# Kernel tuning notes

Hardware: AMD Instinct MI355X
Metric: run time of the kernel (lower is better)

Reference implementation:

```python
import jax, jax.numpy as jnp
import numpy as np

B, T, F, H, C = 256, 128, 256, 512, 10


def setup_inputs() -> dict:
    key = jax.random.key(0)
    ks = jax.random.split(key, 11)
    s_in = 1.0 / np.sqrt(H)  # torch RNN init scale ~ U(-1/sqrt(H), 1/sqrt(H)); use scaled normal
    return {
        "x": jax.random.normal(ks[0], (B, T, F), jnp.float32),
        "W_ih0": jax.random.normal(ks[1], (H, F), jnp.float32) * s_in,
        "W_hh0": jax.random.normal(ks[2], (H, H), jnp.float32) * s_in,
        "b_ih0": jax.random.normal(ks[3], (H,), jnp.float32) * s_in,
        "b_hh0": jax.random.normal(ks[4], (H,), jnp.float32) * s_in,
        "W_ih1": jax.random.normal(ks[5], (H, H), jnp.float32) * s_in,
        "W_hh1": jax.random.normal(ks[6], (H, H), jnp.float32) * s_in,
        "b_ih1": jax.random.normal(ks[7], (H,), jnp.float32) * s_in,
        "b_hh1": jax.random.normal(ks[8], (H,), jnp.float32) * s_in,
        "W_fc": jax.random.normal(ks[9], (C, H * T), jnp.float32) * (1.0 / np.sqrt(H * T)),
        "b_fc": jax.random.normal(ks[10], (C,), jnp.float32) * 0.01,
    }


def _rnn_layer(inp, W_ih, W_hh, b_ih, b_hh):
    # inp: [B, T, Fin]. Precompute all input-to-hidden projections in one GEMM.
    proj = jnp.einsum('btf,hf->bth', inp, W_ih) + b_ih + b_hh  # [B, T, H]

    def step(h, p_t):
        h_new = jax.nn.relu(p_t + h @ W_hh.T)  # h_t = relu(x W_ih^T + b_ih + h_{t-1} W_hh^T + b_hh)
        return h_new, h_new

    h0 = jnp.zeros((inp.shape[0], W_hh.shape[0]), inp.dtype)
    _, outs = jax.lax.scan(step, h0, jnp.swapaxes(proj, 0, 1))  # scan over T
    return jnp.swapaxes(outs, 0, 1)  # [B, T, H]


def reference(x, W_ih0, W_hh0, b_ih0, b_hh0, W_ih1, W_hh1, b_ih1, b_hh1, W_fc, b_fc):
    h = _rnn_layer(x, W_ih0, W_hh0, b_ih0, b_hh0)
    h = _rnn_layer(h, W_ih1, W_hh1, b_ih1, b_hh1)
    flat = h.reshape(h.shape[0], -1)  # [B, T*H]
    return flat @ W_fc.T + b_fc  # [B, C]
```

## Files before the change

kernel.cpp:

```cpp
#include <hip/hip_runtime.h>
#include <cstddef>

#define B_ 256
#define T_ 128
#define F_ 256
#define H_ 512
#define C_ 10

#define TEAMS 32
#define TB    8
#define BS    8
#define NS    64

typedef short bf16x8 __attribute__((ext_vector_type(8)));
typedef float f32x4  __attribute__((ext_vector_type(4)));

__device__ __forceinline__ unsigned short f2bf_rn(float f) {
    unsigned u = __builtin_bit_cast(unsigned, f);
    u += 0x7fffu + ((u >> 16) & 1u);
    return (unsigned short)(u >> 16);
}
__device__ __forceinline__ float bf2f(unsigned short s) {
    unsigned u = (unsigned)s << 16;
    return __builtin_bit_cast(float, u);
}

__global__ __launch_bounds__(256, 2) void gemm_mfma_kernel(
    const float* __restrict__ A, const float* __restrict__ W,
    const float* __restrict__ b1, const float* __restrict__ b2,
    float* __restrict__ Cout)
{
    __shared__ alignas(16) unsigned short Ahi[128 * 32];
    __shared__ alignas(16) unsigned short Alo[128 * 32];
    __shared__ alignas(16) unsigned short Bhi[128 * 32];
    __shared__ alignas(16) unsigned short Blo[128 * 32];

    const int tid  = threadIdx.x;
    const int m0   = blockIdx.x * 128;
    const int n0   = blockIdx.y * 128;
    const int lane = tid & 63;
    const int wv   = tid >> 6;
    const int wr   = (wv >> 1) << 6;
    const int wc   = (wv & 1) << 6;

    f32x4 acc[4][4];
#pragma unroll
    for (int i = 0; i < 4; i++)
#pragma unroll
        for (int j = 0; j < 4; j++) acc[i][j] = f32x4{0.f, 0.f, 0.f, 0.f};

    float bias[4];
#pragma unroll
    for (int ct = 0; ct < 4; ct++) {
        const int n = n0 + wc + ct * 16 + (lane & 15);
        bias[ct] = b1[n] + b2[n];
    }

    const int kcol  = tid & 15;
    const int rbase = tid >> 4;
    const int koct2 = (lane >> 4) << 4;

    for (int k0 = 0; k0 < F_; k0 += 32) {
#pragma unroll
        for (int i = 0; i < 8; i++) {
            const int row = rbase + 16 * i;
            float2 av = *(const float2*)(A + (size_t)(m0 + row) * F_ + k0 + kcol * 2);
            float2 wv2 = *(const float2*)(W + (size_t)(n0 + row) * F_ + k0 + kcol * 2);
            const int addr = ((row << 6) | (kcol << 2)) ^ ((row & 7) << 4);
            unsigned short h0, h1;
            h0 = f2bf_rn(av.x); h1 = f2bf_rn(av.y);
            *(unsigned*)((char*)Ahi + addr) =
                (unsigned)h0 | ((unsigned)h1 << 16);
            *(unsigned*)((char*)Alo + addr) =
                (unsigned)f2bf_rn(av.x - bf2f(h0)) |
                ((unsigned)f2bf_rn(av.y - bf2f(h1)) << 16);
            h0 = f2bf_rn(wv2.x); h1 = f2bf_rn(wv2.y);
            *(unsigned*)((char*)Bhi + addr) =
                (unsigned)h0 | ((unsigned)h1 << 16);
            *(unsigned*)((char*)Blo + addr) =
                (unsigned)f2bf_rn(wv2.x - bf2f(h0)) |
                ((unsigned)f2bf_rn(wv2.y - bf2f(h1)) << 16);
        }
        __syncthreads();

        bf16x8 fah[4], fal[4], fbh[4], fbl[4];
#pragma unroll
        for (int rt = 0; rt < 4; rt++) {
            const int r = wr + rt * 16 + (lane & 15);
            const int addr = ((r << 6) | koct2) ^ ((r & 7) << 4);
            fah[rt] = *(const bf16x8*)((const char*)Ahi + addr);
            fal[rt] = *(const bf16x8*)((const char*)Alo + addr);
        }
#pragma unroll
        for (int ct = 0; ct < 4; ct++) {
            const int c = wc + ct * 16 + (lane & 15);
            const int addr = ((c << 6) | koct2) ^ ((c & 7) << 4);
            fbh[ct] = *(const bf16x8*)((const char*)Bhi + addr);
            fbl[ct] = *(const bf16x8*)((const char*)Blo + addr);
        }
#pragma unroll
        for (int rt = 0; rt < 4; rt++)
#pragma unroll
            for (int ct = 0; ct < 4; ct++) {
                acc[rt][ct] = __builtin_amdgcn_mfma_f32_16x16x32_bf16(
                    fah[rt], fbh[ct], acc[rt][ct], 0, 0, 0);
                acc[rt][ct] = __builtin_amdgcn_mfma_f32_16x16x32_bf16(
                    fah[rt], fbl[ct], acc[rt][ct], 0, 0, 0);
                acc[rt][ct] = __builtin_amdgcn_mfma_f32_16x16x32_bf16(
                    fal[rt], fbh[ct], acc[rt][ct], 0, 0, 0);
            }
        __syncthreads();
    }

#pragma unroll
    for (int rt = 0; rt < 4; rt++) {
        const int m = m0 + wr + rt * 16 + ((lane >> 4) << 2);
#pragma unroll
        for (int ct = 0; ct < 4; ct++) {
            const int n = n0 + wc + ct * 16 + (lane & 15);
#pragma unroll
            for (int q = 0; q < 4; q++)
                Cout[(size_t)(m + q) * H_ + n] = acc[rt][ct][q] + bias[ct];
        }
    }
}

__device__ __forceinline__ void load_wfrag(
    const float* __restrict__ W, int wrow, int khalf, int koct,
    bf16x8* bhi, bf16x8* blo)
{
#pragma unroll
    for (int ks = 0; ks < 8; ks++) {
        const float* wp = W + (size_t)wrow * H_ + khalf + ks * 32 + koct;
        const unsigned long long* q = (const unsigned long long*)wp;
        float f[8];
#pragma unroll
        for (int j = 0; j < 4; j++) {
            union { unsigned long long q; float f[2]; } u;
            u.q = __hip_atomic_load(q + j, __ATOMIC_RELAXED,
                                    __HIP_MEMORY_SCOPE_AGENT);
            f[2 * j] = u.f[0]; f[2 * j + 1] = u.f[1];
        }
#pragma unroll
        for (int j = 0; j < 8; j++) {
            unsigned short hi = f2bf_rn(f[j]);
            unsigned short lo = f2bf_rn(f[j] - bf2f(hi));
            bhi[ks][j] = (short)hi;
            blo[ks][j] = (short)lo;
        }
    }
}

__global__ __launch_bounds__(512, 2) void fused_scan_kernel(
    float* __restrict__ ws0, float* __restrict__ ws1,
    const float* __restrict__ Whh0, const float* __restrict__ Wih1,
    const float* __restrict__ Whh1,
    const float* __restrict__ bih1, const float* __restrict__ bhh1,
    unsigned int* __restrict__ bar)
{
    __shared__ alignas(16) unsigned short hs0_hi[BS * H_];
    __shared__ alignas(16) unsigned short hs0_lo[BS * H_];
    __shared__ alignas(16) unsigned short hs1_hi[BS * H_];
    __shared__ alignas(16) unsigned short hs1_lo[BS * H_];
    __shared__ alignas(16) float red0[8][8][17];
    __shared__ alignas(16) float red1[8][8][17];

    const int tid   = threadIdx.x;
    const int team  = blockIdx.x & 31;
    const int mem   = blockIdx.x >> 5;
    const int b0    = team * BS;
    const int n0    = mem * NS;
    const int lane  = tid & 63;
    const int wv    = tid >> 6;
    const int ct    = wv >> 1;
    const int khalf = (wv & 1) << 8;

    unsigned int* cnt = bar + team * 16;

    const int wrow = n0 + (ct << 4) + (lane & 15);
    const int koct = (lane >> 4) << 3;
    bf16x8 w0hi[8], w0lo[8], wihi[8], wilo[8], w1hi[8], w1lo[8];
    load_wfrag(Whh0, wrow, khalf, koct, w0hi, w0lo);
    load_wfrag(Wih1, wrow, khalf, koct, wihi, wilo);
    load_wfrag(Whh1, wrow, khalf, koct, w1hi, w1lo);

    const int bb = tid >> 6;
    const int cc = tid & 63;
    float* p0 = ws0 + ((size_t)(b0 + bb) * T_) * H_ + n0 + cc;
    float* p1 = ws1 + ((size_t)(b0 + bb) * T_) * H_ + n0 + cc;
    float projv = *p0;
    const float bias1v = bih1[n0 + cc] + bhh1[n0 + cc];

    const int qw    = tid & 255;
    const int rhalf = (tid >> 8) * 4;

    const int arow  = lane & 7;
    const int rbase = arow << 10;
    const int kxor  = arow << 4;
    const int klane = (lane >> 4) << 4;

    for (int r = 0; r <= T_; r++) {
        if (r == 0) {
            ((float4*)hs0_hi)[tid] = float4{0.f, 0.f, 0.f, 0.f};
            ((float4*)hs0_lo)[tid] = float4{0.f, 0.f, 0.f, 0.f};
        } else {
            const float* sp = ws0 + ((size_t)b0 * T_ + (r - 1)) * H_;
#pragma unroll
            for (int i = 0; i < 4; i++) {
                const int b = rhalf + i;
                unsigned long long v = __hip_atomic_load(
                    (const unsigned long long*)(sp + (size_t)b * T_ * H_) + qw,
                    __ATOMIC_RELAXED, __HIP_MEMORY_SCOPE_AGENT);
                union { unsigned long long q; float f[2]; } u; u.q = v;
                unsigned short h0 = f2bf_rn(u.f[0]);
                unsigned short h1 = f2bf_rn(u.f[1]);
                unsigned short l0 = f2bf_rn(u.f[0] - bf2f(h0));
                unsigned short l1 = f2bf_rn(u.f[1] - bf2f(h1));
                const int addr = ((b << 10) | (qw << 2)) ^ (b << 4);
                *(unsigned int*)((char*)hs0_hi + addr) =
                    (unsigned int)h0 | ((unsigned int)h1 << 16);
                *(unsigned int*)((char*)hs0_lo + addr) =
                    (unsigned int)l0 | ((unsigned int)l1 << 16);
            }
        }
        if (r <= 1) {
            ((float4*)hs1_hi)[tid] = float4{0.f, 0.f, 0.f, 0.f};
            ((float4*)hs1_lo)[tid] = float4{0.f, 0.f, 0.f, 0.f};
        } else {
            const float* sp = ws1 + ((size_t)b0 * T_ + (r - 2)) * H_;
#pragma unroll
            for (int i = 0; i < 4; i++) {
                const int b = rhalf + i;
                unsigned long long v = __hip_atomic_load(
                    (const unsigned long long*)(sp + (size_t)b * T_ * H_) + qw,
                    __ATOMIC_RELAXED, __HIP_MEMORY_SCOPE_AGENT);
                union { unsigned long long q; float f[2]; } u; u.q = v;
                unsigned short h0 = f2bf_rn(u.f[0]);
                unsigned short h1 = f2bf_rn(u.f[1]);
                unsigned short l0 = f2bf_rn(u.f[0] - bf2f(h0));
                unsigned short l1 = f2bf_rn(u.f[1] - bf2f(h1));
                const int addr = ((b << 10) | (qw << 2)) ^ (b << 4);
                *(unsigned int*)((char*)hs1_hi + addr) =
                    (unsigned int)h0 | ((unsigned int)h1 << 16);
                *(unsigned int*)((char*)hs1_lo + addr) =
                    (unsigned int)l0 | ((unsigned int)l1 << 16);
            }
        }
        __syncthreads();

        f32x4 a0x = {0.f,0.f,0.f,0.f}, a0y = {0.f,0.f,0.f,0.f};
        f32x4 a1x = {0.f,0.f,0.f,0.f}, a1y = {0.f,0.f,0.f,0.f};
#pragma unroll
        for (int ks = 0; ks < 8; ks++) {
            const int kbyte = (khalf << 1) + ks * 64 + klane;
            const int addr  = rbase | (kbyte ^ kxor);
            bf16x8 h0hi = *(const bf16x8*)((const char*)hs0_hi + addr);
            bf16x8 h0lo = *(const bf16x8*)((const char*)hs0_lo + addr);
            bf16x8 h1hi = *(const bf16x8*)((const char*)hs1_hi + addr);
            bf16x8 h1lo = *(const bf16x8*)((const char*)hs1_lo + addr);
            if ((ks & 1) == 0) {
                a0x = __builtin_amdgcn_mfma_f32_16x16x32_bf16(h0hi, w0hi[ks], a0x, 0, 0, 0);
                a0x = __builtin_amdgcn_mfma_f32_16x16x32_bf16(h0hi, w0lo[ks], a0x, 0, 0, 0);
                a0x = __builtin_amdgcn_mfma_f32_16x16x32_bf16(h0lo, w0hi[ks], a0x, 0, 0, 0);
                a1x = __builtin_amdgcn_mfma_f32_16x16x32_bf16(h0hi, wihi[ks], a1x, 0, 0, 0);
                a1x = __builtin_amdgcn_mfma_f32_16x16x32_bf16(h0hi, wilo[ks], a1x, 0, 0, 0);
                a1x = __builtin_amdgcn_mfma_f32_16x16x32_bf16(h0lo, wihi[ks], a1x, 0, 0, 0);
                a1x = __builtin_amdgcn_mfma_f32_16x16x32_bf16(h1hi, w1hi[ks], a1x, 0, 0, 0);
                a1x = __builtin_amdgcn_mfma_f32_16x16x32_bf16(h1hi, w1lo[ks], a1x, 0, 0, 0);
                a1x = __builtin_amdgcn_mfma_f32_16x16x32_bf16(h1lo, w1hi[ks], a1x, 0, 0, 0);
            } else {
                a0y = __builtin_amdgcn_mfma_f32_16x16x32_bf16(h0hi, w0hi[ks], a0y, 0, 0, 0);
                a0y = __builtin_amdgcn_mfma_f32_16x16x32_bf16(h0hi, w0lo[ks], a0y, 0, 0, 0);
                a0y = __builtin_amdgcn_mfma_f32_16x16x32_bf16(h0lo, w0hi[ks], a0y, 0, 0, 0);
                a1y = __builtin_amdgcn_mfma_f32_16x16x32_bf16(h0hi, wihi[ks], a1y, 0, 0, 0);
                a1y = __builtin_amdgcn_mfma_f32_16x16x32_bf16(h0hi, wilo[ks], a1y, 0, 0, 0);
                a1y = __builtin_amdgcn_mfma_f32_16x16x32_bf16(h0lo, wihi[ks], a1y, 0, 0, 0);
                a1y = __builtin_amdgcn_mfma_f32_16x16x32_bf16(h1hi, w1hi[ks], a1y, 0, 0, 0);
                a1y = __builtin_amdgcn_mfma_f32_16x16x32_bf16(h1hi, w1lo[ks], a1y, 0, 0, 0);
                a1y = __builtin_amdgcn_mfma_f32_16x16x32_bf16(h1lo, w1hi[ks], a1y, 0, 0, 0);
            }
        }

        if (lane < 32) {
            const int rrow = (lane >> 4) << 2;
            const int col  = lane & 15;
#pragma unroll
            for (int q = 0; q < 4; q++) {
                red0[wv][rrow + q][col] = a0x[q] + a0y[q];
                red1[wv][rrow + q][col] = a1x[q] + a1y[q];
            }
        }
        __syncthreads();

        {
            const int wv0 = (cc >> 4) << 1;
            const int ci  = cc & 15;
            if (r < T_) {
                float s0 = red0[wv0][bb][ci] + red0[wv0 + 1][bb][ci];
                float h  = fmaxf(s0 + projv, 0.f);
                __hip_atomic_store(p0 + (size_t)r * H_, h,
                                   __ATOMIC_RELAXED, __HIP_MEMORY_SCOPE_AGENT);
            }
            if (r >= 1) {
                float s1 = red1[wv0][bb][ci] + red1[wv0 + 1][bb][ci];
                float h  = fmaxf(s1 + bias1v, 0.f);
                __hip_atomic_store(p1 + (size_t)(r - 1) * H_, h,
                                   __ATOMIC_RELAXED, __HIP_MEMORY_SCOPE_AGENT);
            }
        }

        if (r < T_) {
            __syncthreads();
            if (tid == 0)
                __hip_atomic_fetch_add(cnt, 1u,
                                       __ATOMIC_RELAXED, __HIP_MEMORY_SCOPE_AGENT);
            float nextproj = 0.f;
            if (r + 1 < T_)
                nextproj = p0[(size_t)(r + 1) * H_];
            if (tid == 0) {
                const unsigned target = (unsigned)TB * (unsigned)(r + 1);
                while (__hip_atomic_load(cnt, __ATOMIC_RELAXED,
                                         __HIP_MEMORY_SCOPE_AGENT) < target) {
                    __builtin_amdgcn_s_sleep(1);
                }
            }
            __syncthreads();
            projv = nextproj;
        }
    }
}

__global__ __launch_bounds__(256) void fc_kernel(
    const float* __restrict__ Hl, const float* __restrict__ Wfc,
    const float* __restrict__ bfc, float* __restrict__ out)
{
    const int b = blockIdx.x;
    const int tid = threadIdx.x;
    const float* hb = Hl + (size_t)b * (T_ * H_);

    float acc[C_];
#pragma unroll
    for (int c = 0; c < C_; c++) acc[c] = 0.f;

    for (int i = tid * 4; i < T_ * H_; i += 256 * 4) {
        float4 hv = *(const float4*)(hb + i);
#pragma unroll
        for (int c = 0; c < C_; c++) {
            float4 wv = *(const float4*)(Wfc + (size_t)c * (T_ * H_) + i);
            acc[c] = fmaf(hv.x, wv.x, fmaf(hv.y, wv.y,
                     fmaf(hv.z, wv.z, fmaf(hv.w, wv.w, acc[c]))));
        }
    }

    __shared__ float red[4][C_];
#pragma unroll
    for (int c = 0; c < C_; c++) {
        float v = acc[c];
#pragma unroll
        for (int off = 32; off >= 1; off >>= 1) v += __shfl_xor(v, off, 64);
        if ((tid & 63) == 0) red[tid >> 6][c] = v;
    }
    __syncthreads();
    if (tid < C_) {
        float v = red[0][tid] + red[1][tid] + red[2][tid] + red[3][tid] + bfc[tid];
        out[(size_t)b * C_ + tid] = v;
    }
}

extern "C" void kernel_launch(void* const* d_in, const int* in_sizes, int n_in,
                              void* d_out, int out_size, void* d_ws, size_t ws_size,
                              hipStream_t stream)
{
    (void)in_sizes; (void)n_in; (void)out_size; (void)ws_size;

    const float* x    = (const float*)d_in[0];
    const float* Wih0 = (const float*)d_in[1];
    const float* Whh0 = (const float*)d_in[2];
    const float* bih0 = (const float*)d_in[3];
    const float* bhh0 = (const float*)d_in[4];
    const float* Wih1 = (const float*)d_in[5];
    const float* Whh1 = (const float*)d_in[6];
    const float* bih1 = (const float*)d_in[7];
    const float* bhh1 = (const float*)d_in[8];
    const float* Wfc  = (const float*)d_in[9];
    const float* bfc  = (const float*)d_in[10];
    float* out = (float*)d_out;

    float* ws0 = (float*)d_ws;
    float* ws1 = ws0 + (size_t)B_ * T_ * H_;
    unsigned int* bar = (unsigned int*)d_out;

    hipMemsetAsync(bar, 0, TEAMS * 16 * sizeof(unsigned int), stream);

    dim3 gproj(B_ * T_ / 128, H_ / 128);

    gemm_mfma_kernel<<<gproj, 256, 0, stream>>>(x, Wih0, bih0, bhh0, ws0);
    fused_scan_kernel<<<TEAMS * TB, 512, 0, stream>>>(
        ws0, ws1, Whh0, Wih1, Whh1, bih1, bhh1, bar);
    fc_kernel<<<B_, 256, 0, stream>>>(ws1, Wfc, bfc, out);
}
```

Measured before the change: 797.1 us.

## Fuse final FC projection into scan kernel and move barrier counters to device global

New measurement: 961.8 us. 1.21x slower.

```diff
diff --git a/kernel.cpp b/kernel.cpp
--- a/kernel.cpp
+++ b/kernel.cpp
@@ -14,6 +14,8 @@
 
 typedef short bf16x8 __attribute__((ext_vector_type(8)));
 typedef float f32x4  __attribute__((ext_vector_type(4)));
+
+__device__ __attribute__((aligned(64))) unsigned g_bar[TEAMS * 16];
 
 __device__ __forceinline__ unsigned short f2bf_rn(float f) {
     unsigned u = __builtin_bit_cast(unsigned, f);
@@ -36,6 +38,12 @@
     __shared__ alignas(16) unsigned short Blo[128 * 32];
 
     const int tid  = threadIdx.x;
+
+    if (blockIdx.x == 0 && blockIdx.y == 0) {
+        g_bar[tid] = 0;
+        g_bar[tid + 256] = 0;
+    }
+
     const int m0   = blockIdx.x * 128;
     const int n0   = blockIdx.y * 128;
     const int lane = tid & 63;
@@ -151,12 +159,13 @@
     }
 }
 
-__global__ __launch_bounds__(512, 2) void fused_scan_kernel(
+__global__ __launch_bounds__(512, 1) void fused_scan_kernel(
     float* __restrict__ ws0, float* __restrict__ ws1,
     const float* __restrict__ Whh0, const float* __restrict__ Wih1,
     const float* __restrict__ Whh1,
     const float* __restrict__ bih1, const float* __restrict__ bhh1,
-    unsigned int* __restrict__ bar)
+    const float* __restrict__ Wfc, const float* __restrict__ bfc,
+    float* __restrict__ out)
 {
     __shared__ alignas(16) unsigned short hs0_hi[BS * H_];
     __shared__ alignas(16) unsigned short hs0_lo[BS * H_];
@@ -175,7 +184,7 @@
     const int ct    = wv >> 1;
     const int khalf = (wv & 1) << 8;
 
-    unsigned int* cnt = bar + team * 16;
+    unsigned int* cnt = g_bar + team * 16;
 
     const int wrow = n0 + (ct << 4) + (lane & 15);
     const int koct = (lane >> 4) << 3;
@@ -190,6 +199,11 @@
     float* p1 = ws1 + ((size_t)(b0 + bb) * T_) * H_ + n0 + cc;
     float projv = *p0;
     const float bias1v = bih1[n0 + cc] + bhh1[n0 + cc];
+
+    float accfc[C_];
+#pragma unroll
+    for (int c = 0; c < C_; c++) accfc[c] = 0.f;
+    const float* wfc0 = Wfc + n0 + cc;
 
     const int qw    = tid & 255;
     const int rhalf = (tid >> 8) * 4;
@@ -292,6 +306,7 @@
         }
         __syncthreads();
 
+        float h1v = 0.f;
         {
             const int wv0 = (cc >> 4) << 1;
             const int ci  = cc & 15;
@@ -303,8 +318,8 @@
             }
             if (r >= 1) {
                 float s1 = red1[wv0][bb][ci] + red1[wv0 + 1][bb][ci];
-                float h  = fmaxf(s1 + bias1v, 0.f);
-                __hip_atomic_store(p1 + (size_t)(r - 1) * H_, h,
+                h1v = fmaxf(s1 + bias1v, 0.f);
+                __hip_atomic_store(p1 + (size_t)(r - 1) * H_, h1v,
                                    __ATOMIC_RELAXED, __HIP_MEMORY_SCOPE_AGENT);
             }
         }
@@ -314,6 +329,12 @@
             if (tid == 0)
                 __hip_atomic_fetch_add(cnt, 1u,
                                        __ATOMIC_RELAXED, __HIP_MEMORY_SCOPE_AGENT);
+            if (r >= 1) {
+                const float* wp = wfc0 + (size_t)(r - 1) * H_;
+#pragma unroll
+                for (int c = 0; c < C_; c++)
+                    accfc[c] = fmaf(h1v, wp[(size_t)c * (T_ * H_)], accfc[c]);
+            }
             float nextproj = 0.f;
             if (r + 1 < T_)
                 nextproj = p0[(size_t)(r + 1) * H_];
@@ -326,44 +347,23 @@
             }
             __syncthreads();
             projv = nextproj;
-        }
-    }
-}
-
-__global__ __launch_bounds__(256) void fc_kernel(
-    const float* __restrict__ Hl, const float* __restrict__ Wfc,
-    const float* __restrict__ bfc, float* __restrict__ out)
-{
-    const int b = blockIdx.x;
-    const int tid = threadIdx.x;
-    const float* hb = Hl + (size_t)b * (T_ * H_);
-
-    float acc[C_];
-#pragma unroll
-    for (int c = 0; c < C_; c++) acc[c] = 0.f;
-
-    for (int i = tid * 4; i < T_ * H_; i += 256 * 4) {
-        float4 hv = *(const float4*)(hb + i);
-#pragma unroll
-        for (int c = 0; c < C_; c++) {
-            float4 wv = *(const float4*)(Wfc + (size_t)c * (T_ * H_) + i);
-            acc[c] = fmaf(hv.x, wv.x, fmaf(hv.y, wv.y,
-                     fmaf(hv.z, wv.z, fmaf(hv.w, wv.w, acc[c]))));
-        }
-    }
-
-    __shared__ float red[4][C_];
+        } else {
+            const float* wp = wfc0 + (size_t)(T_ - 1) * H_;
+#pragma unroll
+            for (int c = 0; c < C_; c++)
+                accfc[c] = fmaf(h1v, wp[(size_t)c * (T_ * H_)], accfc[c]);
+        }
+    }
+
 #pragma unroll
     for (int c = 0; c < C_; c++) {
-        float v = acc[c];
+        float v = accfc[c];
 #pragma unroll
         for (int off = 32; off >= 1; off >>= 1) v += __shfl_xor(v, off, 64);
-        if ((tid & 63) == 0) red[tid >> 6][c] = v;
-    }
-    __syncthreads();
-    if (tid < C_) {
-        float v = red[0][tid] + red[1][tid] + red[2][tid] + red[3][tid] + bfc[tid];
-        out[(size_t)b * C_ + tid] = v;
+        if (lane == 0) {
+            if (mem == 0) v += bfc[c];
+            atomicAdd(out + (size_t)(b0 + bb) * C_ + c, v);
+        }
     }
 }
 
@@ -388,14 +388,12 @@
 
     float* ws0 = (float*)d_ws;
     float* ws1 = ws0 + (size_t)B_ * T_ * H_;
-    unsigned int* bar = (unsigned int*)d_out;
-
-    hipMemsetAsync(bar, 0, TEAMS * 16 * sizeof(unsigned int), stream);
+
+    hipMemsetAsync(out, 0, (size_t)B_ * C_ * sizeof(float), stream);
 
     dim3 gproj(B_ * T_ / 128, H_ / 128);
 
     gemm_mfma_kernel<<<gproj, 256, 0, stream>>>(x, Wih0, bih0, bhh0, ws0);
     fused_scan_kernel<<<TEAMS * TB, 512, 0, stream>>>(
-        ws0, ws1, Whh0, Wih1, Whh1, bih1, bhh1, bar);
-    fc_kernel<<<B_, 256, 0, stream>>>(ws1, Wfc, bfc, out);
-}
+        ws0, ws1, Whh0, Wih1, Whh1, bih1, bhh1, Wfc, bfc, out);
+}
```
